# Performance work log

Hardware: AMD Instinct MI355X
Metric: run time of the kernel (lower is better)

Reference implementation:

```python
import jax, jax.numpy as jnp
import numpy as np

B, T, D = 2, 2048, 1024
N_HEADS, N_KV_HEADS = 16, 4
D_HEAD = D // N_HEADS            # 64
N_GROUPS = N_HEADS // N_KV_HEADS  # 4
ROPE_THETA = 10000.0


def _rope_freqs(t, d_head, theta):
    inv = 1.0 / (theta ** (jnp.arange(0, d_head, 2, dtype=jnp.float32) / d_head))  # (d_head/2,)
    ang = jnp.arange(t, dtype=jnp.float32)[:, None] * inv[None, :]                 # (T, d_head/2)
    return jnp.stack([jnp.cos(ang), jnp.sin(ang)], axis=-1)                        # (T, d_head/2, 2)


def _apply_rope(x, freqs):
    # x: (B, T, H, d_head); freqs: (T, d_head/2, 2) = (cos, sin)
    xr = x.reshape(*x.shape[:-1], -1, 2)          # (B,T,H,d/2,2)
    xre, xim = xr[..., 0], xr[..., 1]
    fre = freqs[None, :, None, :, 0]              # (1,T,1,d/2)
    fim = freqs[None, :, None, :, 1]
    outre = xre * fre - xim * fim
    outim = xre * fim + xim * fre
    return jnp.stack([outre, outim], axis=-1).reshape(x.shape)


def setup_inputs() -> dict:
    key = jax.random.key(0)
    ks = jax.random.split(key, 5)
    x = jax.random.normal(ks[0], (B, T, D), dtype=jnp.float32)
    w_q = jax.random.normal(ks[1], (N_HEADS * D_HEAD, D), dtype=jnp.float32) * 0.02
    w_k = jax.random.normal(ks[2], (N_KV_HEADS * D_HEAD, D), dtype=jnp.float32) * 0.02
    w_v = jax.random.normal(ks[3], (N_KV_HEADS * D_HEAD, D), dtype=jnp.float32) * 0.02
    w_o = jax.random.normal(ks[4], (D, N_HEADS * D_HEAD), dtype=jnp.float32) * 0.02
    rope_freqs = _rope_freqs(T, D_HEAD, ROPE_THETA)
    causal = jnp.tril(jnp.ones((T, T), dtype=bool))
    mask = jnp.where(causal, 0.0, -1e9).astype(jnp.float32)[None, None]  # (1,1,T,T)
    return {"x": x, "rope_freqs": rope_freqs, "mask": mask,
            "w_q": w_q, "w_k": w_k, "w_v": w_v, "w_o": w_o}


def reference(x, rope_freqs, mask, w_q, w_k, w_v, w_o):
    # projections (torch Linear: y = x @ W.T)
    q = jnp.einsum('btd,od->bto', x, w_q).reshape(B, T, N_HEADS, D_HEAD)
    k = jnp.einsum('btd,od->bto', x, w_k).reshape(B, T, N_KV_HEADS, D_HEAD)
    v = jnp.einsum('btd,od->bto', x, w_v).reshape(B, T, N_KV_HEADS, D_HEAD)
    q = _apply_rope(q, rope_freqs)
    k = _apply_rope(k, rope_freqs)
    # GQA: expand KV heads (kv head h -> N_GROUPS contiguous query heads)
    k = jnp.repeat(k, N_GROUPS, axis=2)   # (B,T,H,d)
    v = jnp.repeat(v, N_GROUPS, axis=2)
    q = q.transpose(0, 2, 1, 3)           # (B,H,T,d)
    k = k.transpose(0, 2, 1, 3)
    v = v.transpose(0, 2, 1, 3)
    scale = 1.0 / np.sqrt(D_HEAD).astype(np.float32)
    scores = jnp.einsum('bhqd,bhkd->bhqk', q, k) * scale + mask
    attn = jax.nn.softmax(scores, axis=-1)
    out = jnp.einsum('bhqk,bhkd->bhqd', attn, v)
    out = out.transpose(0, 2, 1, 3).reshape(B, T, N_HEADS * D_HEAD)
    return jnp.einsum('bto,do->btd', out, w_o)
```

## Files before the change

### kernel.cpp

```cpp
#include <hip/hip_runtime.h>
#include <hip/hip_bf16.h>
#include <cstddef>
#include <type_traits>

#define TT   2048
#define NH   16
#define NKV  4
#define DH   64

typedef __bf16 bf16x8 __attribute__((ext_vector_type(8)));
typedef float  f32x4  __attribute__((ext_vector_type(4)));

#if __has_builtin(__builtin_amdgcn_exp2f)
#define EXP2F(x) __builtin_amdgcn_exp2f(x)
#else
#define EXP2F(x) __expf((x) * 0.69314718056f)
#endif

#define QSCALE 0.180336880f

__global__ __launch_bounds__(256)
void cast_kernel(const float* __restrict__ x,  const float* __restrict__ wq,
                 const float* __restrict__ wk, const float* __restrict__ wv,
                 const float* __restrict__ wo,
                 __bf16* __restrict__ xb, __bf16* __restrict__ wqkv,
                 __bf16* __restrict__ wob)
{
    const int g = blockIdx.x * 256 + threadIdx.x;
    const float* src;
    __bf16* dst;
    int off;
    if (g < 1048576)       { src = x;  dst = xb;   off = g; }
    else if (g < 1310720)  { src = wq; dst = wqkv; off = g - 1048576; }
    else if (g < 1376256)  { src = wk; dst = wqkv + 1048576; off = g - 1310720; }
    else if (g < 1441792)  { src = wv; dst = wqkv + 1310720; off = g - 1376256; }
    else                   { src = wo; dst = wob;  off = g - 1441792; }
    const float4 v = *(const float4*)(src + (size_t)off * 4);
    union { __bf16 h[4]; uint2 u; } o;
    o.h[0] = (__bf16)v.x; o.h[1] = (__bf16)v.y;
    o.h[2] = (__bf16)v.z; o.h[3] = (__bf16)v.w;
    *(uint2*)(dst + (size_t)off * 4) = o.u;
}

template<int MODE>
__global__ __launch_bounds__(256, 3)
void mm_kernel(const __bf16* __restrict__ A,
               const __bf16* __restrict__ W,
               const float* __restrict__ rope,
               void* __restrict__ O0, void* __restrict__ O1,
               void* __restrict__ O2)
{
    constexpr int K  = 1024;
    constexpr int NK = K / 64;
    constexpr int NX = (MODE == 0) ? 12 : 8;
    __shared__ __bf16 As[2][64 * 64];
    __shared__ __bf16 Bs[2][128 * 64];

    const int tid  = threadIdx.x;
    const int lane = tid & 63;
    const int wv   = tid >> 6;
    const int quad = lane >> 4;
    const int lc   = lane & 15;

    const int dlin = blockIdx.x + NX * blockIdx.y;
    const int nid  = (dlin & 7) * ((NX * 64) >> 3) + (dlin >> 3);
    const int bx   = nid % NX;
    const int by   = nid / NX;

    const int gm0  = by * 64;
    const int gn0  = bx * 128;
    const int wc0  = wv * 32;

    size_t gaA[2]; int lsA[2];
#pragma unroll
    for (int j = 0; j < 2; j++) {
        const int p = tid + j * 256;
        const int r = p >> 3, g = (p & 7) ^ (r & 7);
        gaA[j] = (size_t)r * K + g * 8;
        lsA[j] = p * 8;
    }
    size_t gaB[4]; int lsB[4];
#pragma unroll
    for (int j = 0; j < 4; j++) {
        const int p = tid + j * 256;
        const int r = p >> 3, g = (p & 7) ^ (r & 7);
        gaB[j] = (size_t)r * K + g * 8;
        lsB[j] = p * 8;
    }
    const __bf16* Ag = A + (size_t)gm0 * K;
    const __bf16* Wg = W + (size_t)gn0 * K;

    int aoff[4][2], boff[2][2];
#pragma unroll
    for (int i = 0; i < 4; i++)
#pragma unroll
        for (int kk = 0; kk < 2; kk++)
            aoff[i][kk] = ((i * 16 + lc) * 8 + ((kk * 4 + quad) ^ (lc & 7))) * 8;
#pragma unroll
    for (int j = 0; j < 2; j++)
#pragma unroll
        for (int kk = 0; kk < 2; kk++)
            boff[j][kk] = ((wc0 + j * 16 + lc) * 8 + ((kk * 4 + quad) ^ (lc & 7))) * 8;

    f32x4 acc[4][2];
#pragma unroll
    for (int i = 0; i < 4; i++)
#pragma unroll
        for (int j = 0; j < 2; j++) acc[i][j] = (f32x4){0.f, 0.f, 0.f, 0.f};

    bf16x8 ar[2][2], br[2][4];

    auto load_set = [&](int kt, int s) {
        const int kb = kt * 64;
#pragma unroll
        for (int j = 0; j < 2; j++) ar[s][j] = *(const bf16x8*)(Ag + gaA[j] + kb);
#pragma unroll
        for (int j = 0; j < 4; j++) br[s][j] = *(const bf16x8*)(Wg + gaB[j] + kb);
    };
    auto store_set = [&](int s) {
#pragma unroll
        for (int j = 0; j < 2; j++) *(bf16x8*)&As[s][lsA[j]] = ar[s][j];
#pragma unroll
        for (int j = 0; j < 4; j++) *(bf16x8*)&Bs[s][lsB[j]] = br[s][j];
    };

    load_set(0, 0);
    store_set(0);
    load_set(1, 1);
    load_set(2, 0);
    __syncthreads();

    auto step = [&](int kt, auto pc) {
        constexpr int P = decltype(pc)::value;
        constexpr int Q = 1 - P;
        bf16x8 af[4][2], bfr[2][2];
#pragma unroll
        for (int i = 0; i < 4; i++)
#pragma unroll
            for (int kk = 0; kk < 2; kk++)
                af[i][kk] = *(const bf16x8*)&As[P][aoff[i][kk]];
#pragma unroll
        for (int j = 0; j < 2; j++)
#pragma unroll
            for (int kk = 0; kk < 2; kk++)
                bfr[j][kk] = *(const bf16x8*)&Bs[P][boff[j][kk]];
        if (kt + 1 < NK) store_set(Q);
#pragma unroll
        for (int kk = 0; kk < 2; kk++)
#pragma unroll
            for (int i = 0; i < 4; i++)
#pragma unroll
                for (int j = 0; j < 2; j++)
                    acc[i][j] = __builtin_amdgcn_mfma_f32_16x16x32_bf16(
                        af[i][kk], bfr[j][kk], acc[i][j], 0, 0, 0);
        if (kt + 3 < NK) load_set(kt + 3, Q);
        if (kt + 1 < NK) __syncthreads();
    };
    for (int kt = 0; kt < NK; kt += 2) {
        step(kt,     std::integral_constant<int, 0>{});
        step(kt + 1, std::integral_constant<int, 1>{});
    }

    if (MODE == 0) {
        __bf16* Qo = (__bf16*)O0;
        __bf16* Ko = (__bf16*)O1;
        __bf16* Vo = (__bf16*)O2;
        const int region = (gn0 < 1024) ? 0 : (gn0 < 1280) ? 1 : 2;
#pragma unroll
        for (int i = 0; i < 4; i++) {
#pragma unroll
            for (int r = 0; r < 4; r++) {
                const int grow = gm0 + i * 16 + quad * 4 + r;
                const int b = grow >> 11, t = grow & 2047;
                const float* rrow = rope + t * 64;
#pragma unroll
                for (int j = 0; j < 2; j++) {
                    const float v = acc[i][j][r];
                    const float partner = __shfl_xor(v, 1, 64);
                    const int col = gn0 + wc0 + j * 16 + lc;
                    if (region == 0) {
                        const int h = col >> 6, d = col & 63;
                        const float2 cs = *(const float2*)(rrow + (d >> 1) * 2);
                        const float out = v * cs.x + partner * ((d & 1) ? cs.y : -cs.y);
                        Qo[((size_t)(b * NH + h) * TT + t) * DH + d] = (__bf16)(out * QSCALE);
                    } else if (region == 1) {
                        const int ck = col - 1024;
                        const int kh = ck >> 6, d = ck & 63;
                        const float2 cs = *(const float2*)(rrow + (d >> 1) * 2);
                        const float out = v * cs.x + partner * ((d & 1) ? cs.y : -cs.y);
                        Ko[((size_t)(b * NKV + kh) * TT + t) * DH + d] = (__bf16)out;
                    } else {
                        const int cv = col - 1280;
                        const int kh = cv >> 6, d = cv & 63;
                        Vo[((size_t)(b * NKV + kh) * DH + d) * TT + t] = (__bf16)v;
                    }
                }
            }
        }
    } else {
        float* Of = (float*)O0;
#pragma unroll
        for (int i = 0; i < 4; i++)
#pragma unroll
            for (int r = 0; r < 4; r++) {
                const int grow = gm0 + i * 16 + quad * 4 + r;
#pragma unroll
                for (int j = 0; j < 2; j++)
                    Of[(size_t)grow * 1024 + gn0 + wc0 + j * 16 + lc] = acc[i][j][r];
            }
    }
}

__global__ __launch_bounds__(256, 4)
void attn_kernel(const __bf16* __restrict__ Q,
                 const __bf16* __restrict__ K,
                 const __bf16* __restrict__ Vt,
                 __bf16* __restrict__ O)
{
    __shared__ __bf16 Ks[2][64 * 64];
    __shared__ __bf16 Vs[2][64 * 64];
    __shared__ __bf16 Ps[4][16][64];

    const int tid  = threadIdx.x;
    const int lane = tid & 63;
    const int wv   = tid >> 6;
    const int quad = lane >> 4;
    const int lc   = lane & 15;

    const int a   = blockIdx.x & 31;
    const int rep = blockIdx.x >> 5;
    const int qt  = ((rep >> 3) & 1) ? (31 - a) : a;
    const int b   = rep >> 4;
    const int h   = rep & 15;
    const int kh  = h >> 2;
    const int nk  = qt + 1;

    const __bf16* Kg = K  + (size_t)(b * NKV + kh) * TT * DH;
    const __bf16* Vg = Vt + (size_t)(b * NKV + kh) * DH * TT;

    bf16x8 qb[2];
    {
        const __bf16* qp = Q + ((size_t)(b * NH + h) * TT
                                + qt * 64 + wv * 16 + lc) * DH;
        qb[0] = *(const bf16x8*)(qp + quad * 8);
        qb[1] = *(const bf16x8*)(qp + 32 + quad * 8);
    }

    int koff[2], voff[2], lsl[2];
#pragma unroll
    for (int j = 0; j < 2; j++) {
        const int p  = tid + j * 256;
        const int r  = p >> 3;
        const int qs = (p & 7) ^ (r & 7);
        koff[j] = r * DH + qs * 8;
        voff[j] = r * TT + qs * 8;
        lsl[j]  = p * 8;
    }

    int foff[4][2];
#pragma unroll
    for (int g = 0; g < 4; g++)
#pragma unroll
        for (int c = 0; c < 2; c++)
            foff[g][c] = ((g * 16 + lc) * 8 + ((c * 4 + quad) ^ (lc & 7))) * 8;

    const int psw = 2 * (lc & 7);
    char* prow = (char*)&Ps[wv][lc][0];

    float l_s = 0.f;
    f32x4 oacc[4];
#pragma unroll
    for (int g = 0; g < 4; g++) oacc[g] = (f32x4){0.f, 0.f, 0.f, 0.f};

    bf16x8 kr[2], vr[2];
    auto load_regs = [&](int kt) {
        const __bf16* kp = Kg + (size_t)kt * 64 * DH;
        const __bf16* vp = Vg + (size_t)kt * 64;
#pragma unroll
        for (int j = 0; j < 2; j++) {
            kr[j] = *(const bf16x8*)(kp + koff[j]);
            vr[j] = *(const bf16x8*)(vp + voff[j]);
        }
    };
    auto store_lds = [&](int buf) {
#pragma unroll
        for (int j = 0; j < 2; j++) {
            *(bf16x8*)&Ks[buf][lsl[j]] = kr[j];
            *(bf16x8*)&Vs[buf][lsl[j]] = vr[j];
        }
    };

    load_regs(0);
    store_lds(0);
    if (nk > 1) load_regs(1);
    __syncthreads();

    for (int kt = 0; kt < nk; kt++) {
        const int cur = kt & 1;

        bf16x8 ka[4][2];
#pragma unroll
        for (int g = 0; g < 4; g++) {
            ka[g][0] = *(const bf16x8*)&Ks[cur][foff[g][0]];
            ka[g][1] = *(const bf16x8*)&Ks[cur][foff[g][1]];
        }

        if (kt + 1 < nk) store_lds(cur ^ 1);

        const int D = qt * 64 + wv * 16 - kt * 64;

        f32x4 s[4];
        __builtin_amdgcn_s_setprio(1);
#pragma unroll
        for (int g = 0; g < 4; g++) {
            f32x4 z = (f32x4){0.f, 0.f, 0.f, 0.f};
            z = __builtin_amdgcn_mfma_f32_16x16x32_bf16(ka[g][0], qb[0], z, 0, 0, 0);
            z = __builtin_amdgcn_mfma_f32_16x16x32_bf16(ka[g][1], qb[1], z, 0, 0, 0);
            s[g] = z;
        }
        __builtin_amdgcn_s_setprio(0);

        if (D < 63) {
            const int thr = D + lc;
#pragma unroll
            for (int g = 0; g < 4; g++)
#pragma unroll
                for (int r = 0; r < 4; r++)
                    if (g * 16 + quad * 4 + r > thr) s[g][r] = -1e30f;
        }

        float rs = 0.f;
#pragma unroll
        for (int g = 0; g < 4; g++) {
#pragma unroll
            for (int r = 0; r < 4; r++) {
                s[g][r] = EXP2F(s[g][r]);
                rs += s[g][r];
            }
            union { __bf16 hh[4]; uint2 uu; } pk;
            pk.hh[0] = (__bf16)s[g][0]; pk.hh[1] = (__bf16)s[g][1];
            pk.hh[2] = (__bf16)s[g][2]; pk.hh[3] = (__bf16)s[g][3];
            *(uint2*)(prow + ((4 * g + quad) ^ psw) * 8) = pk.uu;
        }
        l_s += rs;

        bf16x8 va[4][2];
#pragma unroll
        for (int g = 0; g < 4; g++) {
            va[g][0] = *(const bf16x8*)&Vs[cur][foff[g][0]];
            va[g][1] = *(const bf16x8*)&Vs[cur][foff[g][1]];
        }

        const bf16x8 pb0 = *(const bf16x8*)(prow + (( 2 * quad) ^ psw) * 8);
        const bf16x8 pb1 = *(const bf16x8*)(prow + ((8 + 2 * quad) ^ psw) * 8);
        __builtin_amdgcn_s_setprio(1);
#pragma unroll
        for (int g = 0; g < 4; g++) {
            oacc[g] = __builtin_amdgcn_mfma_f32_16x16x32_bf16(va[g][0], pb0, oacc[g], 0, 0, 0);
            oacc[g] = __builtin_amdgcn_mfma_f32_16x16x32_bf16(va[g][1], pb1, oacc[g], 0, 0, 0);
        }
        __builtin_amdgcn_s_setprio(0);

        if (kt + 2 < nk) load_regs(kt + 2);
        if (kt + 1 < nk) __syncthreads();
    }

    {
        float l = l_s;
        l += __shfl_xor(l, 16, 64);
        l += __shfl_xor(l, 32, 64);
        const float inv = 1.f / l;
        const int t = qt * 64 + wv * 16 + lc;
        __bf16* op = O + (size_t)(b * TT + t) * (NH * DH) + h * DH;
#pragma unroll
        for (int g = 0; g < 4; g++) {
            union { __bf16 hh[4]; uint2 uu; } pk;
            pk.hh[0] = (__bf16)(oacc[g][0] * inv);
            pk.hh[1] = (__bf16)(oacc[g][1] * inv);
            pk.hh[2] = (__bf16)(oacc[g][2] * inv);
            pk.hh[3] = (__bf16)(oacc[g][3] * inv);
            *(uint2*)(op + g * 16 + quad * 4) = pk.uu;
        }
    }
}

extern "C" void kernel_launch(void* const* d_in, const int* in_sizes, int n_in,
                              void* d_out, int out_size, void* d_ws, size_t ws_size,
                              hipStream_t stream)
{
    const float* x    = (const float*)d_in[0];
    const float* rope = (const float*)d_in[1];
    const float* w_q  = (const float*)d_in[3];
    const float* w_k  = (const float*)d_in[4];
    const float* w_v  = (const float*)d_in[5];
    const float* w_o  = (const float*)d_in[6];
    float* out = (float*)d_out;

    char* ws = (char*)d_ws;
    __bf16* Qb   = (__bf16*)(ws);
    __bf16* Kb   = (__bf16*)(ws + (8  << 20));
    __bf16* Vtb  = (__bf16*)(ws + (10 << 20));
    __bf16* AOb  = (__bf16*)(ws + (12 << 20));
    __bf16* xb   = (__bf16*)(ws + (20 << 20));
    __bf16* Wqkv = (__bf16*)(ws + (28 << 20));
    __bf16* Wob  = (__bf16*)(ws + (31 << 20));

    cast_kernel<<<6656, dim3(256), 0, stream>>>(x, w_q, w_k, w_v, w_o,
                                                xb, Wqkv, Wob);

    dim3 g1(12, 64);
    mm_kernel<0><<<g1, dim3(256), 0, stream>>>(xb, Wqkv, rope,
                                               (void*)Qb, (void*)Kb, (void*)Vtb);

    attn_kernel<<<1024, dim3(256), 0, stream>>>(Qb, Kb, Vtb, AOb);

    dim3 g3(8, 64);
    mm_kernel<1><<<g3, dim3(256), 0, stream>>>(AOb, Wob, rope,
                                               (void*)out, nullptr, nullptr);
}
```

Before: 171.0 us.

## Load K and V tiles directly from global memory, dropping LDS staging

The attention kernel no longer stages K and V tiles through double-buffered shared memory with swizzled offsets. Each wave now reads its MFMA operands straight from global memory (through the cache) every iteration, which removes the LDS stores, the LDS reads and the per-tile __syncthreads. The cost is that all four waves fetch the same K/V data redundantly and the register prefetch pipeline is gone, so global-load latency is exposed on every iteration.

After: 250.6 us. +46.5%, slower.

```diff
diff --git a/kernel.cpp b/kernel.cpp
--- a/kernel.cpp
+++ b/kernel.cpp
@@ -217,8 +217,6 @@
                  const __bf16* __restrict__ Vt,
                  __bf16* __restrict__ O)
 {
-    __shared__ __bf16 Ks[2][64 * 64];
-    __shared__ __bf16 Vs[2][64 * 64];
     __shared__ __bf16 Ps[4][16][64];
 
     const int tid  = threadIdx.x;
@@ -246,23 +244,8 @@
         qb[1] = *(const bf16x8*)(qp + 32 + quad * 8);
     }
 
-    int koff[2], voff[2], lsl[2];
-#pragma unroll
-    for (int j = 0; j < 2; j++) {
-        const int p  = tid + j * 256;
-        const int r  = p >> 3;
-        const int qs = (p & 7) ^ (r & 7);
-        koff[j] = r * DH + qs * 8;
-        voff[j] = r * TT + qs * 8;
-        lsl[j]  = p * 8;
-    }
-
-    int foff[4][2];
-#pragma unroll
-    for (int g = 0; g < 4; g++)
-#pragma unroll
-        for (int c = 0; c < 2; c++)
-            foff[g][c] = ((g * 16 + lc) * 8 + ((c * 4 + quad) ^ (lc & 7))) * 8;
+    const __bf16* kbase = Kg + (size_t)lc * DH + quad * 8;
+    const __bf16* vbase = Vg + (size_t)lc * TT + quad * 8;
 
     const int psw = 2 * (lc & 7);
     char* prow = (char*)&Ps[wv][lc][0];
@@ -272,40 +255,21 @@
 #pragma unroll
     for (int g = 0; g < 4; g++) oacc[g] = (f32x4){0.f, 0.f, 0.f, 0.f};
 
-    bf16x8 kr[2], vr[2];
-    auto load_regs = [&](int kt) {
-        const __bf16* kp = Kg + (size_t)kt * 64 * DH;
-        const __bf16* vp = Vg + (size_t)kt * 64;
-#pragma unroll
-        for (int j = 0; j < 2; j++) {
-            kr[j] = *(const bf16x8*)(kp + koff[j]);
-            vr[j] = *(const bf16x8*)(vp + voff[j]);
-        }
-    };
-    auto store_lds = [&](int buf) {
-#pragma unroll
-        for (int j = 0; j < 2; j++) {
-            *(bf16x8*)&Ks[buf][lsl[j]] = kr[j];
-            *(bf16x8*)&Vs[buf][lsl[j]] = vr[j];
-        }
-    };
-
-    load_regs(0);
-    store_lds(0);
-    if (nk > 1) load_regs(1);
-    __syncthreads();
-
     for (int kt = 0; kt < nk; kt++) {
-        const int cur = kt & 1;
-
         bf16x8 ka[4][2];
 #pragma unroll
         for (int g = 0; g < 4; g++) {
-            ka[g][0] = *(const bf16x8*)&Ks[cur][foff[g][0]];
-            ka[g][1] = *(const bf16x8*)&Ks[cur][foff[g][1]];
-        }
-
-        if (kt + 1 < nk) store_lds(cur ^ 1);
+            const __bf16* kp = kbase + (size_t)(kt * 64 + g * 16) * DH;
+            ka[g][0] = *(const bf16x8*)(kp);
+            ka[g][1] = *(const bf16x8*)(kp + 32);
+        }
+        bf16x8 va[4][2];
+#pragma unroll
+        for (int g = 0; g < 4; g++) {
+            const __bf16* vp = vbase + (size_t)(g * 16) * TT + kt * 64;
+            va[g][0] = *(const bf16x8*)(vp);
+            va[g][1] = *(const bf16x8*)(vp + 32);
+        }
 
         const int D = qt * 64 + wv * 16 - kt * 64;
 
@@ -344,13 +308,6 @@
         }
         l_s += rs;
 
-        bf16x8 va[4][2];
-#pragma unroll
-        for (int g = 0; g < 4; g++) {
-            va[g][0] = *(const bf16x8*)&Vs[cur][foff[g][0]];
-            va[g][1] = *(const bf16x8*)&Vs[cur][foff[g][1]];
-        }
-
         const bf16x8 pb0 = *(const bf16x8*)(prow + (( 2 * quad) ^ psw) * 8);
         const bf16x8 pb1 = *(const bf16x8*)(prow + ((8 + 2 * quad) ^ psw) * 8);
         __builtin_amdgcn_s_setprio(1);
@@ -360,9 +317,6 @@
             oacc[g] = __builtin_amdgcn_mfma_f32_16x16x32_bf16(va[g][1], pb1, oacc[g], 0, 0, 0);
         }
         __builtin_amdgcn_s_setprio(0);
-
-        if (kt + 2 < nk) load_regs(kt + 2);
-        if (kt + 1 < nk) __syncthreads();
     }
 
     {
```

## Process 128 query rows per attention block to reuse K/V tiles

Applied to the files above, without the earlier changes.

The attention kernel now has each wave handle two 16-row query sub-tiles, so a block covers 128 query rows instead of 64 and the grid shrinks from 1024 to 512 blocks. Each K/V tile loaded into LDS now feeds twice as many MFMAs, which halves global K/V traffic and the per-tile sync overhead per query row. In exchange, register use roughly doubles (launch bounds lowered to 2 blocks per SIMD), there are fewer blocks for causal load balancing, and masked work grows on diagonal tiles.

Measured after the change: 175.8 us. +2.8%, slower.

```diff
diff --git a/kernel.cpp b/kernel.cpp
--- a/kernel.cpp
+++ b/kernel.cpp
@@ -211,7 +211,7 @@
     }
 }
 
-__global__ __launch_bounds__(256, 4)
+__global__ __launch_bounds__(256, 2)
 void attn_kernel(const __bf16* __restrict__ Q,
                  const __bf16* __restrict__ K,
                  const __bf16* __restrict__ Vt,
@@ -219,7 +219,7 @@
 {
     __shared__ __bf16 Ks[2][64 * 64];
     __shared__ __bf16 Vs[2][64 * 64];
-    __shared__ __bf16 Ps[4][16][64];
+    __shared__ __bf16 Ps[4][32][64];
 
     const int tid  = threadIdx.x;
     const int lane = tid & 63;
@@ -227,23 +227,24 @@
     const int quad = lane >> 4;
     const int lc   = lane & 15;
 
-    const int a   = blockIdx.x & 31;
-    const int rep = blockIdx.x >> 5;
-    const int qt  = ((rep >> 3) & 1) ? (31 - a) : a;
+    const int a   = blockIdx.x & 15;
+    const int rep = blockIdx.x >> 4;
+    const int qt  = ((rep >> 3) & 1) ? (15 - a) : a;
     const int b   = rep >> 4;
     const int h   = rep & 15;
     const int kh  = h >> 2;
-    const int nk  = qt + 1;
+    const int nk  = 2 * qt + 2;
 
     const __bf16* Kg = K  + (size_t)(b * NKV + kh) * TT * DH;
     const __bf16* Vg = Vt + (size_t)(b * NKV + kh) * DH * TT;
 
-    bf16x8 qb[2];
-    {
+    bf16x8 qb[2][2];
+#pragma unroll
+    for (int u = 0; u < 2; u++) {
         const __bf16* qp = Q + ((size_t)(b * NH + h) * TT
-                                + qt * 64 + wv * 16 + lc) * DH;
-        qb[0] = *(const bf16x8*)(qp + quad * 8);
-        qb[1] = *(const bf16x8*)(qp + 32 + quad * 8);
+                                + qt * 128 + wv * 32 + u * 16 + lc) * DH;
+        qb[u][0] = *(const bf16x8*)(qp + quad * 8);
+        qb[u][1] = *(const bf16x8*)(qp + 32 + quad * 8);
     }
 
     int koff[2], voff[2], lsl[2];
@@ -265,12 +266,15 @@
             foff[g][c] = ((g * 16 + lc) * 8 + ((c * 4 + quad) ^ (lc & 7))) * 8;
 
     const int psw = 2 * (lc & 7);
-    char* prow = (char*)&Ps[wv][lc][0];
-
-    float l_s = 0.f;
-    f32x4 oacc[4];
-#pragma unroll
-    for (int g = 0; g < 4; g++) oacc[g] = (f32x4){0.f, 0.f, 0.f, 0.f};
+    char* prow0 = (char*)&Ps[wv][lc][0];
+    char* prow1 = (char*)&Ps[wv][16 + lc][0];
+
+    float l_s[2] = {0.f, 0.f};
+    f32x4 oacc[2][4];
+#pragma unroll
+    for (int u = 0; u < 2; u++)
+#pragma unroll
+        for (int g = 0; g < 4; g++) oacc[u][g] = (f32x4){0.f, 0.f, 0.f, 0.f};
 
     bf16x8 kr[2], vr[2];
     auto load_regs = [&](int kt) {
@@ -307,42 +311,50 @@
 
         if (kt + 1 < nk) store_lds(cur ^ 1);
 
-        const int D = qt * 64 + wv * 16 - kt * 64;
-
-        f32x4 s[4];
+        f32x4 s[2][4];
         __builtin_amdgcn_s_setprio(1);
 #pragma unroll
-        for (int g = 0; g < 4; g++) {
-            f32x4 z = (f32x4){0.f, 0.f, 0.f, 0.f};
-            z = __builtin_amdgcn_mfma_f32_16x16x32_bf16(ka[g][0], qb[0], z, 0, 0, 0);
-            z = __builtin_amdgcn_mfma_f32_16x16x32_bf16(ka[g][1], qb[1], z, 0, 0, 0);
-            s[g] = z;
-        }
+        for (int u = 0; u < 2; u++)
+#pragma unroll
+            for (int g = 0; g < 4; g++) {
+                f32x4 z = (f32x4){0.f, 0.f, 0.f, 0.f};
+                z = __builtin_amdgcn_mfma_f32_16x16x32_bf16(ka[g][0], qb[u][0], z, 0, 0, 0);
+                z = __builtin_amdgcn_mfma_f32_16x16x32_bf16(ka[g][1], qb[u][1], z, 0, 0, 0);
+                s[u][g] = z;
+            }
         __builtin_amdgcn_s_setprio(0);
 
-        if (D < 63) {
-            const int thr = D + lc;
-#pragma unroll
-            for (int g = 0; g < 4; g++)
-#pragma unroll
-                for (int r = 0; r < 4; r++)
-                    if (g * 16 + quad * 4 + r > thr) s[g][r] = -1e30f;
-        }
-
-        float rs = 0.f;
-#pragma unroll
-        for (int g = 0; g < 4; g++) {
-#pragma unroll
-            for (int r = 0; r < 4; r++) {
-                s[g][r] = EXP2F(s[g][r]);
-                rs += s[g][r];
-            }
-            union { __bf16 hh[4]; uint2 uu; } pk;
-            pk.hh[0] = (__bf16)s[g][0]; pk.hh[1] = (__bf16)s[g][1];
-            pk.hh[2] = (__bf16)s[g][2]; pk.hh[3] = (__bf16)s[g][3];
-            *(uint2*)(prow + ((4 * g + quad) ^ psw) * 8) = pk.uu;
-        }
-        l_s += rs;
+#pragma unroll
+        for (int u = 0; u < 2; u++) {
+            const int D = qt * 128 + wv * 32 + u * 16 - kt * 64;
+            if (D < 63) {
+                const int thr = D + lc;
+#pragma unroll
+                for (int g = 0; g < 4; g++)
+#pragma unroll
+                    for (int r = 0; r < 4; r++)
+                        if (g * 16 + quad * 4 + r > thr) s[u][g][r] = -1e30f;
+            }
+        }
+
+#pragma unroll
+        for (int u = 0; u < 2; u++) {
+            char* prow = u ? prow1 : prow0;
+            float rs = 0.f;
+#pragma unroll
+            for (int g = 0; g < 4; g++) {
+#pragma unroll
+                for (int r = 0; r < 4; r++) {
+                    s[u][g][r] = EXP2F(s[u][g][r]);
+                    rs += s[u][g][r];
+                }
+                union { __bf16 hh[4]; uint2 uu; } pk;
+                pk.hh[0] = (__bf16)s[u][g][0]; pk.hh[1] = (__bf16)s[u][g][1];
+                pk.hh[2] = (__bf16)s[u][g][2]; pk.hh[3] = (__bf16)s[u][g][3];
+                *(uint2*)(prow + ((4 * g + quad) ^ psw) * 8) = pk.uu;
+            }
+            l_s[u] += rs;
+        }
 
         bf16x8 va[4][2];
 #pragma unroll
@@ -351,34 +363,39 @@
             va[g][1] = *(const bf16x8*)&Vs[cur][foff[g][1]];
         }
 
-        const bf16x8 pb0 = *(const bf16x8*)(prow + (( 2 * quad) ^ psw) * 8);
-        const bf16x8 pb1 = *(const bf16x8*)(prow + ((8 + 2 * quad) ^ psw) * 8);
-        __builtin_amdgcn_s_setprio(1);
-#pragma unroll
-        for (int g = 0; g < 4; g++) {
-            oacc[g] = __builtin_amdgcn_mfma_f32_16x16x32_bf16(va[g][0], pb0, oacc[g], 0, 0, 0);
-            oacc[g] = __builtin_amdgcn_mfma_f32_16x16x32_bf16(va[g][1], pb1, oacc[g], 0, 0, 0);
-        }
-        __builtin_amdgcn_s_setprio(0);
+#pragma unroll
+        for (int u = 0; u < 2; u++) {
+            char* prow = u ? prow1 : prow0;
+            const bf16x8 pb0 = *(const bf16x8*)(prow + (( 2 * quad) ^ psw) * 8);
+            const bf16x8 pb1 = *(const bf16x8*)(prow + ((8 + 2 * quad) ^ psw) * 8);
+            __builtin_amdgcn_s_setprio(1);
+#pragma unroll
+            for (int g = 0; g < 4; g++) {
+                oacc[u][g] = __builtin_amdgcn_mfma_f32_16x16x32_bf16(va[g][0], pb0, oacc[u][g], 0, 0, 0);
+                oacc[u][g] = __builtin_amdgcn_mfma_f32_16x16x32_bf16(va[g][1], pb1, oacc[u][g], 0, 0, 0);
+            }
+            __builtin_amdgcn_s_setprio(0);
+        }
 
         if (kt + 2 < nk) load_regs(kt + 2);
         if (kt + 1 < nk) __syncthreads();
     }
 
-    {
-        float l = l_s;
+#pragma unroll
+    for (int u = 0; u < 2; u++) {
+        float l = l_s[u];
         l += __shfl_xor(l, 16, 64);
         l += __shfl_xor(l, 32, 64);
         const float inv = 1.f / l;
-        const int t = qt * 64 + wv * 16 + lc;
+        const int t = qt * 128 + wv * 32 + u * 16 + lc;
         __bf16* op = O + (size_t)(b * TT + t) * (NH * DH) + h * DH;
 #pragma unroll
         for (int g = 0; g < 4; g++) {
             union { __bf16 hh[4]; uint2 uu; } pk;
-            pk.hh[0] = (__bf16)(oacc[g][0] * inv);
-            pk.hh[1] = (__bf16)(oacc[g][1] * inv);
-            pk.hh[2] = (__bf16)(oacc[g][2] * inv);
-            pk.hh[3] = (__bf16)(oacc[g][3] * inv);
+            pk.hh[0] = (__bf16)(oacc[u][g][0] * inv);
+            pk.hh[1] = (__bf16)(oacc[u][g][1] * inv);
+            pk.hh[2] = (__bf16)(oacc[u][g][2] * inv);
+            pk.hh[3] = (__bf16)(oacc[u][g][3] * inv);
             *(uint2*)(op + g * 16 + quad * 4) = pk.uu;
         }
     }
@@ -412,7 +429,7 @@
     mm_kernel<0><<<g1, dim3(256), 0, stream>>>(xb, Wqkv, rope,
                                                (void*)Qb, (void*)Kb, (void*)Vtb);
 
-    attn_kernel<<<1024, dim3(256), 0, stream>>>(Qb, Kb, Vtb, AOb);
+    attn_kernel<<<512, dim3(256), 0, stream>>>(Qb, Kb, Vtb, AOb);
 
     dim3 g3(8, 64);
     mm_kernel<1><<<g3, dim3(256), 0, stream>>>(AOb, Wob, rope,
```
